# Optimization experiments

Hardware: AMD Instinct MI355X
Metric: run time of the kernel (lower is better)

The kernel has to match this reference:

```python
import jax, jax.numpy as jnp
import numpy as np

B, N, D, W = 4, 4096, 256, 7
K = 2 * W + 1  # 15 taps: positions [i-2w, ..., i]
H = 4 * D
EPS = 1e-5


def layer_norm(x, g, b):
    mu = jnp.mean(x, axis=-1, keepdims=True)
    var = jnp.mean(jnp.square(x - mu), axis=-1, keepdims=True)
    return (x - mu) * jax.lax.rsqrt(var + EPS) * g + b


def setup_inputs() -> dict:
    key = jax.random.key(0)
    ks = jax.random.split(key, 8)
    s = 0.02
    return {
        "x": jax.random.normal(ks[0], (B, N, D), dtype=jnp.float32),
        # w_mix[k] is the DxD block of the (K*D -> D) Linear acting on offset k-2w
        "w_mix": (jax.random.normal(ks[1], (K, D, D), dtype=jnp.float32) * s),
        "b_mix": jnp.zeros((D,), dtype=jnp.float32),
        "g1": jnp.ones((D,), jnp.float32) + 0.1 * jax.random.normal(ks[2], (D,), jnp.float32),
        "b1": 0.1 * jax.random.normal(ks[3], (D,), jnp.float32),
        "w_ff1": jax.random.normal(ks[4], (D, H), dtype=jnp.float32) * s,
        "b_ff1": jnp.zeros((H,), dtype=jnp.float32),
        "w_ff2": jax.random.normal(ks[5], (H, D), dtype=jnp.float32) * s,
        "b_ff2": jnp.zeros((D,), dtype=jnp.float32),
        "g2": jnp.ones((D,), jnp.float32) + 0.1 * jax.random.normal(ks[6], (D,), jnp.float32),
        "b2": 0.1 * jax.random.normal(ks[7], (D,), jnp.float32),
    }


def reference(x, w_mix, b_mix, g1, b1, w_ff1, b_ff1, w_ff2, b_ff2, g2, b2):
    # Causal windowed concat + Linear == causal 1D conv with kernel K=2w+1.
    # torch feats chunk k holds x[i - 2w + k]; conv tap k with left pad 2w
    # sees exactly x[i - 2w + k], so kernel = mix weight reshaped (K, D, D).
    mix = jax.lax.conv_general_dilated(
        x, w_mix, window_strides=(1,), padding=[(2 * W, 0)],
        dimension_numbers=("NWC", "WIO", "NWC"),
    ) + b_mix  # [B, N, D]
    # Dropout is identity in eval mode (reference baseline).
    h = layer_norm(x + mix, g1, b1)
    ff = jnp.dot(jax.nn.gelu(jnp.dot(h, w_ff1) + b_ff1, approximate=False), w_ff2) + b_ff2
    return layer_norm(h + ff, g2, b2)
```

## Files before the change

### kernel.cpp

```cpp
#include <hip/hip_runtime.h>
#include <cstdint>

#define DD     256
#define HH     1024
#define NNSEQ  4096
#define KDIM   3840
#define MT     64
#define XROWS  78
#define XPITCH 264
#define SLOTP  260
#define EPSLN  1e-5f

typedef unsigned short u16;
typedef __attribute__((ext_vector_type(8))) short short8;
typedef __attribute__((ext_vector_type(4))) float f32x4;

#define MFMA(a, b, c) __builtin_amdgcn_mfma_f32_16x16x32_bf16(a, b, c, 0, 0, 0)

__device__ __forceinline__ u16 f2bf(float f) {
  unsigned u = __float_as_uint(f);
  u += 0x7FFF + ((u >> 16) & 1);
  return (u16)(u >> 16);
}
__device__ __forceinline__ float bf2f(u16 s) { return __uint_as_float(((unsigned)s) << 16); }

__global__ __launch_bounds__(256) void k_prep(
    const float* __restrict__ wmix, const float* __restrict__ wff1,
    const float* __restrict__ wff2, u16* __restrict__ wpk,
    u16* __restrict__ w1pk, u16* __restrict__ w2pk)
{
  __shared__ float t[32][257];
  const int b = blockIdx.x, tid = threadIdx.x;

  u16* dst;
  if (b < 120) {
    dst = wpk + (size_t)b * 8192;
    for (int r = 0; r < 32; ++r)
      t[r][tid] = wmix[(size_t)(b * 32 + r) * 256 + tid];
  } else if (b < 152) {
    const int u = b - 120, c2 = u >> 3, s = u & 7;
    dst = w1pk + (size_t)u * 8192;
    for (int r = 0; r < 32; ++r)
      t[r][tid] = wff1[(size_t)(s * 32 + r) * 1024 + c2 * 256 + tid];
  } else {
    const int u = b - 152, c2 = u >> 3, s = u & 7;
    dst = w2pk + (size_t)u * 8192;
    for (int r = 0; r < 32; ++r)
      t[r][tid] = wff2[(size_t)(c2 * 256 + s * 32 + r) * 256 + tid];
  }
  __syncthreads();

  const int l = tid & 63, q = l >> 4, cl = l & 15;
#pragma unroll
  for (int f = 0; f < 4; ++f) {
    const int fi = f * 4 + (tid >> 6);
    const int n = fi * 16 + cl;
    uint4 pk;
    unsigned* p = (unsigned*)&pk;
#pragma unroll
    for (int jj = 0; jj < 4; ++jj)
      p[jj] = (unsigned)f2bf(t[q * 8 + jj * 2][n]) | ((unsigned)f2bf(t[q * 8 + jj * 2 + 1][n]) << 16);
    *(uint4*)&dst[(size_t)fi * 512 + l * 8] = pk;
  }
}

__global__ __launch_bounds__(512) void k_fused(
    const float* __restrict__ x, const u16* __restrict__ wpk,
    const float* __restrict__ bmix, const float* __restrict__ g1,
    const float* __restrict__ b1, const u16* __restrict__ w1pk,
    const float* __restrict__ bf1, const u16* __restrict__ w2pk,
    const float* __restrict__ bf2, const float* __restrict__ g2,
    const float* __restrict__ b2, float* __restrict__ out)
{
  __shared__ u16 bufA[XROWS * XPITCH];
  __shared__ float bufB[64 * SLOTP];
  __shared__ float redS[4][64], redS2[4][64];
  __shared__ float muL[64], invL[64];

  const int tid = threadIdx.x;
  const int wv = tid >> 6, l = tid & 63, q = l >> 4, cl = l & 15;
  const int mg = wv >> 2, ng = wv & 3;
  const long tok0 = (long)blockIdx.x * MT;
  const int n0 = (int)(tok0 & (NNSEQ - 1));

  {
    const int cslot = (tid & 63) * 4;
    for (int r = tid >> 6; r < XROWS; r += 8) {
      const int nloc = n0 - 14 + r;
      float4 v = make_float4(0.f, 0.f, 0.f, 0.f);
      if (nloc >= 0) v = *(const float4*)&x[(tok0 - 14 + r) * DD + cslot];
      uint2 pk;
      pk.x = (unsigned)f2bf(v.x) | ((unsigned)f2bf(v.y) << 16);
      pk.y = (unsigned)f2bf(v.z) | ((unsigned)f2bf(v.w) << 16);
      *(uint2*)&bufA[r * XPITCH + cslot] = pk;
    }
  }
  __syncthreads();

  f32x4 acc[4][4];
#pragma unroll
  for (int nt = 0; nt < 4; ++nt) {
    const float bm = (mg == 0) ? bmix[ng * 64 + nt * 16 + cl] : 0.f;
#pragma unroll
    for (int mt = 0; mt < 4; ++mt) acc[mt][nt] = (f32x4){bm, bm, bm, bm};
  }

  const u16* bbase = wpk + (size_t)(mg * 60) * 8192 + (size_t)(ng * 4) * 512 + (size_t)l * 8;

#define LOAD_A(dst, s_)                                                         \
  {                                                                             \
    const int ks = mg * 60 + (s_);                                              \
    const int xrow = ks >> 3, c0 = (ks & 7) * 32;                               \
    _Pragma("unroll")                                                           \
    for (int mt = 0; mt < 4; ++mt)                                              \
      dst[mt] = *(const short8*)&bufA[(xrow + mt * 16 + cl) * XPITCH + c0 + q * 8]; \
  }
#define LOAD_B(dst, s_)                                                         \
  {                                                                             \
    const u16* bp = bbase + (size_t)(s_) * 8192;                                \
    _Pragma("unroll")                                                           \
    for (int nt = 0; nt < 4; ++nt)                                              \
      dst[nt] = *(const short8*)(bp + nt * 512);                                \
  }

  {
    short8 af[3][4], bfr[3][4];
    LOAD_A(af[0], 0) LOAD_B(bfr[0], 0)
    LOAD_A(af[1], 1) LOAD_B(bfr[1], 1)
    LOAD_A(af[2], 2) LOAD_B(bfr[2], 2)

#pragma unroll 3
    for (int s = 0; s < 60; ++s) {
      const int cur = s % 3;
#pragma unroll
      for (int mt = 0; mt < 4; ++mt)
#pragma unroll
        for (int nt = 0; nt < 4; ++nt)
          acc[mt][nt] = MFMA(af[cur][mt], bfr[cur][nt], acc[mt][nt]);
      if (s + 3 < 60) {
        LOAD_A(af[cur], s + 3)
        LOAD_B(bfr[cur], s + 3)
      }
    }
  }
#undef LOAD_A
#undef LOAD_B

  __syncthreads();
  if (mg == 1) {
#pragma unroll
    for (int mt = 0; mt < 4; ++mt)
#pragma unroll
      for (int nt = 0; nt < 4; ++nt)
#pragma unroll
        for (int reg = 0; reg < 4; ++reg)
          bufB[(mt * 16 + q * 4 + reg) * SLOTP + ng * 64 + nt * 16 + cl] = acc[mt][nt][reg];
  }
  __syncthreads();

  if (mg == 0) {
    float ps[4][4], ps2[4][4];
#pragma unroll
    for (int mt = 0; mt < 4; ++mt)
#pragma unroll
      for (int reg = 0; reg < 4; ++reg) {
        const int row = mt * 16 + q * 4 + reg;
        float s = 0.f, s2 = 0.f;
#pragma unroll
        for (int nt = 0; nt < 4; ++nt) {
          const int col = ng * 64 + nt * 16 + cl;
          const float y = acc[mt][nt][reg] + bufB[row * SLOTP + col]
                        + x[(tok0 + row) * DD + col];
          acc[mt][nt][reg] = y;
          s += y; s2 += y * y;
        }
#pragma unroll
        for (int off = 1; off < 16; off <<= 1) { s += __shfl_xor(s, off, 64); s2 += __shfl_xor(s2, off, 64); }
        ps[mt][reg] = s; ps2[mt][reg] = s2;
      }
    if (cl == 0) {
#pragma unroll
      for (int mt = 0; mt < 4; ++mt)
#pragma unroll
        for (int reg = 0; reg < 4; ++reg) {
          const int row = mt * 16 + q * 4 + reg;
          redS[ng][row] = ps[mt][reg]; redS2[ng][row] = ps2[mt][reg];
        }
    }
  }
  __syncthreads();
  if (tid < 64) {
    const float s  = redS[0][tid] + redS[1][tid] + redS[2][tid] + redS[3][tid];
    const float s2 = redS2[0][tid] + redS2[1][tid] + redS2[2][tid] + redS2[3][tid];
    const float mu = s * (1.f / DD);
    const float var = s2 * (1.f / DD) - mu * mu;
    muL[tid] = mu; invL[tid] = rsqrtf(var + EPSLN);
  }
  __syncthreads();

  if (mg == 0) {
#pragma unroll
    for (int nt = 0; nt < 4; ++nt) {
      const int col = ng * 64 + nt * 16 + cl;
      const float gv = g1[col], bv = b1[col];
#pragma unroll
      for (int mt = 0; mt < 4; ++mt)
#pragma unroll
        for (int reg = 0; reg < 4; ++reg) {
          const int row = mt * 16 + q * 4 + reg;
          const float hv = (acc[mt][nt][reg] - muL[row]) * invL[row] * gv + bv;
          bufA[row * XPITCH + col] = f2bf(hv);
        }
    }
  }
  __syncthreads();

  u16* asb = (u16*)bufB;
  f32x4 acc2[2][4];
#pragma unroll
  for (int nt = 0; nt < 4; ++nt) {
    const float bv = bf2[ng * 64 + nt * 16 + cl];
#pragma unroll
    for (int mt = 0; mt < 2; ++mt) acc2[mt][nt] = (f32x4){bv, bv, bv, bv};
  }

  for (int c = 0; c < 4; ++c) {
    f32x4 acc1[2][4];
#pragma unroll
    for (int nt = 0; nt < 4; ++nt) {
      const float bv = bf1[c * 256 + ng * 64 + nt * 16 + cl];
#pragma unroll
      for (int mt = 0; mt < 2; ++mt) acc1[mt][nt] = (f32x4){bv, bv, bv, bv};
    }
#pragma unroll
    for (int s = 0; s < 8; ++s) {
      short8 a[2], b[4];
#pragma unroll
      for (int mt = 0; mt < 2; ++mt)
        a[mt] = *(const short8*)&bufA[(mg * 32 + mt * 16 + cl) * XPITCH + s * 32 + q * 8];
      const u16* bp = w1pk + (size_t)(c * 8 + s) * 8192 + (size_t)(ng * 4) * 512 + (size_t)l * 8;
#pragma unroll
      for (int nt = 0; nt < 4; ++nt)
        b[nt] = *(const short8*)(bp + nt * 512);
#pragma unroll
      for (int mt = 0; mt < 2; ++mt)
#pragma unroll
        for (int nt = 0; nt < 4; ++nt)
          acc1[mt][nt] = MFMA(a[mt], b[nt], acc1[mt][nt]);
    }
#pragma unroll
    for (int mt = 0; mt < 2; ++mt)
#pragma unroll
      for (int nt = 0; nt < 4; ++nt)
#pragma unroll
        for (int reg = 0; reg < 4; ++reg) {
          const float v = acc1[mt][nt][reg];
          const float g = 0.5f * v * (1.f + erff(v * 0.70710678118654752f));
          asb[(mg * 32 + mt * 16 + q * 4 + reg) * XPITCH + ng * 64 + nt * 16 + cl] = f2bf(g);
        }
    __syncthreads();
#pragma unroll
    for (int s = 0; s < 8; ++s) {
      short8 a[2], b[4];
#pragma unroll
      for (int mt = 0; mt < 2; ++mt)
        a[mt] = *(const short8*)&asb[(mg * 32 + mt * 16 + cl) * XPITCH + s * 32 + q * 8];
      const u16* bp = w2pk + (size_t)(c * 8 + s) * 8192 + (size_t)(ng * 4) * 512 + (size_t)l * 8;
#pragma unroll
      for (int nt = 0; nt < 4; ++nt)
        b[nt] = *(const short8*)(bp + nt * 512);
#pragma unroll
      for (int mt = 0; mt < 2; ++mt)
#pragma unroll
        for (int nt = 0; nt < 4; ++nt)
          acc2[mt][nt] = MFMA(a[mt], b[nt], acc2[mt][nt]);
    }
    __syncthreads();
  }

  {
    float ps[2][4], ps2[2][4];
#pragma unroll
    for (int mt = 0; mt < 2; ++mt)
#pragma unroll
      for (int reg = 0; reg < 4; ++reg) {
        const int row = mg * 32 + mt * 16 + q * 4 + reg;
        float s = 0.f, s2 = 0.f;
#pragma unroll
        for (int nt = 0; nt < 4; ++nt) {
          const int col = ng * 64 + nt * 16 + cl;
          const float y = acc2[mt][nt][reg] + bf2f(bufA[row * XPITCH + col]);
          acc2[mt][nt][reg] = y;
          s += y; s2 += y * y;
        }
#pragma unroll
        for (int off = 1; off < 16; off <<= 1) { s += __shfl_xor(s, off, 64); s2 += __shfl_xor(s2, off, 64); }
        ps[mt][reg] = s; ps2[mt][reg] = s2;
      }
    if (cl == 0) {
#pragma unroll
      for (int mt = 0; mt < 2; ++mt)
#pragma unroll
        for (int reg = 0; reg < 4; ++reg) {
          const int row = mg * 32 + mt * 16 + q * 4 + reg;
          redS[ng][row] = ps[mt][reg]; redS2[ng][row] = ps2[mt][reg];
        }
    }
  }
  __syncthreads();
  if (tid < 64) {
    const float s  = redS[0][tid] + redS[1][tid] + redS[2][tid] + redS[3][tid];
    const float s2 = redS2[0][tid] + redS2[1][tid] + redS2[2][tid] + redS2[3][tid];
    const float mu = s * (1.f / DD);
    const float var = s2 * (1.f / DD) - mu * mu;
    muL[tid] = mu; invL[tid] = rsqrtf(var + EPSLN);
  }
  __syncthreads();

#pragma unroll
  for (int nt = 0; nt < 4; ++nt) {
    const int col = ng * 64 + nt * 16 + cl;
    const float gv = g2[col], bv = b2[col];
#pragma unroll
    for (int mt = 0; mt < 2; ++mt)
#pragma unroll
      for (int reg = 0; reg < 4; ++reg) {
        const int row = mg * 32 + mt * 16 + q * 4 + reg;
        out[(tok0 + row) * DD + col] = (acc2[mt][nt][reg] - muL[row]) * invL[row] * gv + bv;
      }
  }
}

extern "C" void kernel_launch(void* const* d_in, const int* in_sizes, int n_in,
                              void* d_out, int out_size, void* d_ws, size_t ws_size,
                              hipStream_t stream) {
  const float* x    = (const float*)d_in[0];
  const float* wmix = (const float*)d_in[1];
  const float* bmix = (const float*)d_in[2];
  const float* g1   = (const float*)d_in[3];
  const float* b1   = (const float*)d_in[4];
  const float* wff1 = (const float*)d_in[5];
  const float* bff1 = (const float*)d_in[6];
  const float* wff2 = (const float*)d_in[7];
  const float* bff2 = (const float*)d_in[8];
  const float* g2   = (const float*)d_in[9];
  const float* b2   = (const float*)d_in[10];
  float* out = (float*)d_out;

  u16* wpk  = (u16*)d_ws;
  u16* w1pk = wpk + 983040;
  u16* w2pk = w1pk + 262144;

  k_prep<<<184, 256, 0, stream>>>(wmix, wff1, wff2, wpk, w1pk, w2pk);

  k_fused<<<256, 512, 0, stream>>>(x, wpk, bmix, g1, b1,
                                   w1pk, bff1, w2pk, bff2, g2, b2, out);
}
```

Baseline: 160.3 us.

## Halve token tile to 32 rows and double grid to fill all CUs

Shrinks the per-block token tile from 64 to 32 rows, so the grid grows from 256 to 512 blocks and covers the MI355X's 256 CUs at least twice. The conv stage keeps its K-split across two wave groups. In the FFN stage each of the 8 waves now owns a 32-column slice of all 32 rows instead of a 2x4 row/column split. The software pipeline depth drops from 3 to 2 and launch bounds request 4 blocks per CU to raise occupancy. In exchange, every weight byte is fetched twice as often per token, and the smaller per-wave MFMA tiles get less data reuse per load.

```diff
diff --git a/kernel.cpp b/kernel.cpp
--- a/kernel.cpp
+++ b/kernel.cpp
@@ -4,9 +4,8 @@
 #define DD     256
 #define HH     1024
 #define NNSEQ  4096
-#define KDIM   3840
-#define MT     64
-#define XROWS  78
+#define MT     32
+#define XR     46
 #define XPITCH 264
 #define SLOTP  260
 #define EPSLN  1e-5f
@@ -64,7 +63,7 @@
   }
 }
 
-__global__ __launch_bounds__(512) void k_fused(
+__global__ __launch_bounds__(512, 4) void k_fused(
     const float* __restrict__ x, const u16* __restrict__ wpk,
     const float* __restrict__ bmix, const float* __restrict__ g1,
     const float* __restrict__ b1, const u16* __restrict__ w1pk,
@@ -72,10 +71,10 @@
     const float* __restrict__ bf2, const float* __restrict__ g2,
     const float* __restrict__ b2, float* __restrict__ out)
 {
-  __shared__ u16 bufA[XROWS * XPITCH];
-  __shared__ float bufB[64 * SLOTP];
-  __shared__ float redS[4][64], redS2[4][64];
-  __shared__ float muL[64], invL[64];
+  __shared__ u16 bufA[XR * XPITCH];
+  __shared__ float bufB[MT * SLOTP];
+  __shared__ float redS[8][MT], redS2[8][MT];
+  __shared__ float muL[MT], invL[MT];
 
   const int tid = threadIdx.x;
   const int wv = tid >> 6, l = tid & 63, q = l >> 4, cl = l & 15;
@@ -85,7 +84,7 @@
 
   {
     const int cslot = (tid & 63) * 4;
-    for (int r = tid >> 6; r < XROWS; r += 8) {
+    for (int r = tid >> 6; r < XR; r += 8) {
       const int nloc = n0 - 14 + r;
       float4 v = make_float4(0.f, 0.f, 0.f, 0.f);
       if (nloc >= 0) v = *(const float4*)&x[(tok0 - 14 + r) * DD + cslot];
@@ -97,12 +96,12 @@
   }
   __syncthreads();
 
-  f32x4 acc[4][4];
+  f32x4 acc[2][4];
 #pragma unroll
   for (int nt = 0; nt < 4; ++nt) {
     const float bm = (mg == 0) ? bmix[ng * 64 + nt * 16 + cl] : 0.f;
 #pragma unroll
-    for (int mt = 0; mt < 4; ++mt) acc[mt][nt] = (f32x4){bm, bm, bm, bm};
+    for (int mt = 0; mt < 2; ++mt) acc[mt][nt] = (f32x4){bm, bm, bm, bm};
   }
 
   const u16* bbase = wpk + (size_t)(mg * 60) * 8192 + (size_t)(ng * 4) * 512 + (size_t)l * 8;
@@ -112,7 +111,7 @@
     const int ks = mg * 60 + (s_);                                              \
     const int xrow = ks >> 3, c0 = (ks & 7) * 32;                               \
     _Pragma("unroll")                                                           \
-    for (int mt = 0; mt < 4; ++mt)                                              \
+    for (int mt = 0; mt < 2; ++mt)                                              \
       dst[mt] = *(const short8*)&bufA[(xrow + mt * 16 + cl) * XPITCH + c0 + q * 8]; \
   }
 #define LOAD_B(dst, s_)                                                         \
@@ -124,22 +123,21 @@
   }
 
   {
-    short8 af[3][4], bfr[3][4];
+    short8 af[2][2], bfr[2][4];
     LOAD_A(af[0], 0) LOAD_B(bfr[0], 0)
     LOAD_A(af[1], 1) LOAD_B(bfr[1], 1)
-    LOAD_A(af[2], 2) LOAD_B(bfr[2], 2)
-
-#pragma unroll 3
+
+#pragma unroll 2
     for (int s = 0; s < 60; ++s) {
-      const int cur = s % 3;
-#pragma unroll
-      for (int mt = 0; mt < 4; ++mt)
+      const int cur = s & 1;
+#pragma unroll
+      for (int mt = 0; mt < 2; ++mt)
 #pragma unroll
         for (int nt = 0; nt < 4; ++nt)
           acc[mt][nt] = MFMA(af[cur][mt], bfr[cur][nt], acc[mt][nt]);
-      if (s + 3 < 60) {
-        LOAD_A(af[cur], s + 3)
-        LOAD_B(bfr[cur], s + 3)
+      if (s + 2 < 60) {
+        LOAD_A(af[cur], s + 2)
+        LOAD_B(bfr[cur], s + 2)
       }
     }
   }
@@ -149,7 +147,7 @@
   __syncthreads();
   if (mg == 1) {
 #pragma unroll
-    for (int mt = 0; mt < 4; ++mt)
+    for (int mt = 0; mt < 2; ++mt)
 #pragma unroll
       for (int nt = 0; nt < 4; ++nt)
 #pragma unroll
@@ -159,9 +157,9 @@
   __syncthreads();
 
   if (mg == 0) {
-    float ps[4][4], ps2[4][4];
-#pragma unroll
-    for (int mt = 0; mt < 4; ++mt)
+    float ps[2][4], ps2[2][4];
+#pragma unroll
+    for (int mt = 0; mt < 2; ++mt)
 #pragma unroll
       for (int reg = 0; reg < 4; ++reg) {
         const int row = mt * 16 + q * 4 + reg;
@@ -180,7 +178,7 @@
       }
     if (cl == 0) {
 #pragma unroll
-      for (int mt = 0; mt < 4; ++mt)
+      for (int mt = 0; mt < 2; ++mt)
 #pragma unroll
         for (int reg = 0; reg < 4; ++reg) {
           const int row = mt * 16 + q * 4 + reg;
@@ -189,7 +187,7 @@
     }
   }
   __syncthreads();
-  if (tid < 64) {
+  if (tid < MT) {
     const float s  = redS[0][tid] + redS[1][tid] + redS[2][tid] + redS[3][tid];
     const float s2 = redS2[0][tid] + redS2[1][tid] + redS2[2][tid] + redS2[3][tid];
     const float mu = s * (1.f / DD);
@@ -204,7 +202,7 @@
       const int col = ng * 64 + nt * 16 + cl;
       const float gv = g1[col], bv = b1[col];
 #pragma unroll
-      for (int mt = 0; mt < 4; ++mt)
+      for (int mt = 0; mt < 2; ++mt)
 #pragma unroll
         for (int reg = 0; reg < 4; ++reg) {
           const int row = mt * 16 + q * 4 + reg;
@@ -216,63 +214,63 @@
   __syncthreads();
 
   u16* asb = (u16*)bufB;
-  f32x4 acc2[2][4];
-#pragma unroll
-  for (int nt = 0; nt < 4; ++nt) {
-    const float bv = bf2[ng * 64 + nt * 16 + cl];
+  f32x4 acc2[2][2];
+#pragma unroll
+  for (int nt = 0; nt < 2; ++nt) {
+    const float bv = bf2[wv * 32 + nt * 16 + cl];
 #pragma unroll
     for (int mt = 0; mt < 2; ++mt) acc2[mt][nt] = (f32x4){bv, bv, bv, bv};
   }
 
   for (int c = 0; c < 4; ++c) {
-    f32x4 acc1[2][4];
-#pragma unroll
-    for (int nt = 0; nt < 4; ++nt) {
-      const float bv = bf1[c * 256 + ng * 64 + nt * 16 + cl];
+    f32x4 acc1[2][2];
+#pragma unroll
+    for (int nt = 0; nt < 2; ++nt) {
+      const float bv = bf1[c * 256 + wv * 32 + nt * 16 + cl];
 #pragma unroll
       for (int mt = 0; mt < 2; ++mt) acc1[mt][nt] = (f32x4){bv, bv, bv, bv};
     }
 #pragma unroll
     for (int s = 0; s < 8; ++s) {
-      short8 a[2], b[4];
-#pragma unroll
-      for (int mt = 0; mt < 2; ++mt)
-        a[mt] = *(const short8*)&bufA[(mg * 32 + mt * 16 + cl) * XPITCH + s * 32 + q * 8];
-      const u16* bp = w1pk + (size_t)(c * 8 + s) * 8192 + (size_t)(ng * 4) * 512 + (size_t)l * 8;
-#pragma unroll
-      for (int nt = 0; nt < 4; ++nt)
+      short8 a[2], b[2];
+#pragma unroll
+      for (int mt = 0; mt < 2; ++mt)
+        a[mt] = *(const short8*)&bufA[(mt * 16 + cl) * XPITCH + s * 32 + q * 8];
+      const u16* bp = w1pk + (size_t)(c * 8 + s) * 8192 + (size_t)(wv * 2) * 512 + (size_t)l * 8;
+#pragma unroll
+      for (int nt = 0; nt < 2; ++nt)
         b[nt] = *(const short8*)(bp + nt * 512);
 #pragma unroll
       for (int mt = 0; mt < 2; ++mt)
 #pragma unroll
-        for (int nt = 0; nt < 4; ++nt)
+        for (int nt = 0; nt < 2; ++nt)
           acc1[mt][nt] = MFMA(a[mt], b[nt], acc1[mt][nt]);
     }
 #pragma unroll
     for (int mt = 0; mt < 2; ++mt)
 #pragma unroll
-      for (int nt = 0; nt < 4; ++nt)
+      for (int nt = 0; nt < 2; ++nt)
 #pragma unroll
         for (int reg = 0; reg < 4; ++reg) {
           const float v = acc1[mt][nt][reg];
           const float g = 0.5f * v * (1.f + erff(v * 0.70710678118654752f));
-          asb[(mg * 32 + mt * 16 + q * 4 + reg) * XPITCH + ng * 64 + nt * 16 + cl] = f2bf(g);
+          asb[(mt * 16 + q * 4 + reg) * XPITCH + wv * 32 + nt * 16 + cl] = f2bf(g);
         }
     __syncthreads();
 #pragma unroll
     for (int s = 0; s < 8; ++s) {
-      short8 a[2], b[4];
-#pragma unroll
-      for (int mt = 0; mt < 2; ++mt)
-        a[mt] = *(const short8*)&asb[(mg * 32 + mt * 16 + cl) * XPITCH + s * 32 + q * 8];
-      const u16* bp = w2pk + (size_t)(c * 8 + s) * 8192 + (size_t)(ng * 4) * 512 + (size_t)l * 8;
-#pragma unroll
-      for (int nt = 0; nt < 4; ++nt)
+      short8 a[2], b[2];
+#pragma unroll
+      for (int mt = 0; mt < 2; ++mt)
+        a[mt] = *(const short8*)&asb[(mt * 16 + cl) * XPITCH + s * 32 + q * 8];
+      const u16* bp = w2pk + (size_t)(c * 8 + s) * 8192 + (size_t)(wv * 2) * 512 + (size_t)l * 8;
+#pragma unroll
+      for (int nt = 0; nt < 2; ++nt)
         b[nt] = *(const short8*)(bp + nt * 512);
 #pragma unroll
       for (int mt = 0; mt < 2; ++mt)
 #pragma unroll
-        for (int nt = 0; nt < 4; ++nt)
+        for (int nt = 0; nt < 2; ++nt)
           acc2[mt][nt] = MFMA(a[mt], b[nt], acc2[mt][nt]);
     }
     __syncthreads();
@@ -284,11 +282,11 @@
     for (int mt = 0; mt < 2; ++mt)
 #pragma unroll
       for (int reg = 0; reg < 4; ++reg) {
-        const int row = mg * 32 + mt * 16 + q * 4 + reg;
+        const int row = mt * 16 + q * 4 + reg;
         float s = 0.f, s2 = 0.f;
 #pragma unroll
-        for (int nt = 0; nt < 4; ++nt) {
-          const int col = ng * 64 + nt * 16 + cl;
+        for (int nt = 0; nt < 2; ++nt) {
+          const int col = wv * 32 + nt * 16 + cl;
           const float y = acc2[mt][nt][reg] + bf2f(bufA[row * XPITCH + col]);
           acc2[mt][nt][reg] = y;
           s += y; s2 += y * y;
@@ -302,15 +300,16 @@
       for (int mt = 0; mt < 2; ++mt)
 #pragma unroll
         for (int reg = 0; reg < 4; ++reg) {
-          const int row = mg * 32 + mt * 16 + q * 4 + reg;
-          redS[ng][row] = ps[mt][reg]; redS2[ng][row] = ps2[mt][reg];
-        }
-    }
-  }
-  __syncthreads();
-  if (tid < 64) {
-    const float s  = redS[0][tid] + redS[1][tid] + redS[2][tid] + redS[3][tid];
-    const float s2 = redS2[0][tid] + redS2[1][tid] + redS2[2][tid] + redS2[3][tid];
+          const int row = mt * 16 + q * 4 + reg;
+          redS[wv][row] = ps[mt][reg]; redS2[wv][row] = ps2[mt][reg];
+        }
+    }
+  }
+  __syncthreads();
+  if (tid < MT) {
+    float s = 0.f, s2 = 0.f;
+#pragma unroll
+    for (int k = 0; k < 8; ++k) { s += redS[k][tid]; s2 += redS2[k][tid]; }
     const float mu = s * (1.f / DD);
     const float var = s2 * (1.f / DD) - mu * mu;
     muL[tid] = mu; invL[tid] = rsqrtf(var + EPSLN);
@@ -318,14 +317,14 @@
   __syncthreads();
 
 #pragma unroll
-  for (int nt = 0; nt < 4; ++nt) {
-    const int col = ng * 64 + nt * 16 + cl;
+  for (int nt = 0; nt < 2; ++nt) {
+    const int col = wv * 32 + nt * 16 + cl;
     const float gv = g2[col], bv = b2[col];
 #pragma unroll
     for (int mt = 0; mt < 2; ++mt)
 #pragma unroll
       for (int reg = 0; reg < 4; ++reg) {
-        const int row = mg * 32 + mt * 16 + q * 4 + reg;
+        const int row = mt * 16 + q * 4 + reg;
         out[(tok0 + row) * DD + col] = (acc2[mt][nt][reg] - muL[row]) * invL[row] * gv + bv;
       }
   }
@@ -353,6 +352,6 @@
 
   k_prep<<<184, 256, 0, stream>>>(wmix, wff1, wff2, wpk, w1pk, w2pk);
 
-  k_fused<<<256, 512, 0, stream>>>(x, wpk, bmix, g1, b1,
+  k_fused<<<512, 512, 0, stream>>>(x, wpk, bmix, g1, b1,
                                    w1pk, bff1, w2pk, bff2, g2, b2, out);
 }
```

Result: faster. 155.3 us (-3.1%).
